# Optimization experiments

Hardware: AMD Instinct MI355X
Metric: run time of the kernel (lower is better)

## Reference

```python
import jax, jax.numpy as jnp
import numpy as np

N_NODES = 20000
N_EDGES = 400000
IN_DIM = 512
OUT_DIM = 1
HIDDEN = [512, 512, 512, 256, OUT_DIM]


def _glorot(key, fan_in, fan_out):
    lim = np.sqrt(6.0 / (fan_in + fan_out)).astype(np.float32)
    return jax.random.uniform(key, (fan_in, fan_out), jnp.float32, -lim, lim)


def setup_inputs() -> dict:
    key = jax.random.key(0)
    ks = jax.random.split(key, 16)
    x = jax.random.normal(ks[0], (N_NODES, IN_DIM), jnp.float32)
    edge_index = jax.random.randint(ks[1], (2, N_EDGES), 0, N_NODES, jnp.int64)
    edge_attr = jax.random.uniform(ks[2], (N_EDGES,), jnp.float32)
    inp = {"x": x, "edge_index": edge_index, "edge_attr": edge_attr}
    dims = [IN_DIM] + HIDDEN
    for i in range(5):
        inp[f"W{i+1}"] = _glorot(ks[3 + i], dims[i], dims[i + 1])
        inp[f"b{i+1}"] = jnp.zeros((dims[i + 1],), jnp.float32)
    return inp


def gcn_layer(x, W, b, src, dst, ew, n):
    # x: [N, Fin] -> [N, Fout]; GCNConv: D^{-1/2}(A+I)D^{-1/2} X W + b
    h = x @ W
    loop = jnp.arange(n)
    src_f = jnp.concatenate([src, loop])
    dst_f = jnp.concatenate([dst, loop])
    ew_f = jnp.concatenate([ew, jnp.ones((n,), x.dtype)])  # self-loop weight 1
    deg = jax.ops.segment_sum(ew_f, dst_f, num_segments=n)
    dinv = jnp.where(deg > 0, jax.lax.rsqrt(deg), 0.0)
    norm = dinv[src_f] * ew_f * dinv[dst_f]  # [E+N]
    out = jax.ops.segment_sum(norm[:, None] * h[src_f], dst_f, num_segments=n)
    return out + b


def reference(x, edge_index, edge_attr, W1, b1, W2, b2, W3, b3, W4, b4, W5, b5):
    src, dst = edge_index[0], edge_index[1]
    n = x.shape[0]
    h = jax.nn.relu(gcn_layer(x, W1, b1, src, dst, edge_attr, n))
    h = jax.nn.relu(gcn_layer(h, W2, b2, src, dst, edge_attr, n))
    h = jax.nn.relu(gcn_layer(h, W3, b3, src, dst, edge_attr, n))
    h = jax.nn.relu(gcn_layer(h, W4, b4, src, dst, edge_attr, n))
    h = gcn_layer(h, W5, b5, src, dst, edge_attr, n)
    return h
```

## Files before the change

### kernel.cpp

```cpp
#include <hip/hip_runtime.h>
#include <cstdint>
#include <cstddef>

#define N_NODES 20000
#define N_EDGES 400000
#define NBLK 79
#define MPAD 20128

typedef __attribute__((ext_vector_type(8))) short bf16x8;
typedef __attribute__((ext_vector_type(4))) float f32x4;

__device__ __forceinline__ float bf2f(unsigned short u) {
    return __uint_as_float(((unsigned int)u) << 16);
}
__device__ __forceinline__ unsigned short f2bf(float f) {
    unsigned int x = __float_as_uint(f);
    unsigned int lsb = (x >> 16) & 1u;
    x += 0x7fffu + lsb;
    return (unsigned short)(x >> 16);
}

__device__ __forceinline__ float ldF(const void* p, size_t i, bool bf) {
    return bf ? bf2f(((const unsigned short*)p)[i]) : ((const float*)p)[i];
}

__device__ __forceinline__ void gl2lds16(const unsigned short* g, unsigned short* l) {
    __builtin_amdgcn_global_load_lds(
        (const __attribute__((address_space(1))) void*)g,
        (__attribute__((address_space(3))) void*)l, 16, 0, 0);
}

__global__ void k_detect(const unsigned int* __restrict__ xw, const int* __restrict__ raw,
                         int* __restrict__ flag) {
    int lane = threadIdx.x;
    int cnt = 0, nz = 0;
    for (int i = lane; i < 256; i += 64) {
        unsigned short lo = (unsigned short)(xw[i] & 0xffffu);
        int e = (lo >> 7) & 0xff;
        if (e >= 110 && e <= 135) cnt++;
    }
    for (int i = 2 * lane + 1; i < 512; i += 128)
        if (raw[i] != 0) nz++;
#pragma unroll
    for (int off = 32; off > 0; off >>= 1) {
        cnt += __shfl_down(cnt, off);
        nz  += __shfl_down(nz, off);
    }
    if (lane == 0) {
        flag[0] = (cnt >= 128) ? 1 : 0;
        flag[1] = (nz == 0) ? 1 : 0;
    }
}

__global__ void k_canon_deg(const int* __restrict__ raw, const void* __restrict__ ew,
                            const int* __restrict__ flagp,
                            int* __restrict__ src32, int* __restrict__ dst32,
                            float* __restrict__ deg, int* __restrict__ counts) {
    bool bf = (flagp[0] != 0);
    int is64 = flagp[1];
    int e = blockIdx.x * blockDim.x + threadIdx.x;
    if (e >= N_EDGES) return;
    int s, d;
    if (is64) { s = raw[2 * e]; d = raw[2 * (N_EDGES + e)]; }
    else      { s = raw[e];     d = raw[N_EDGES + e]; }
    src32[e] = s;
    dst32[e] = d;
    atomicAdd(&deg[d], ldF(ew, e, bf));
    atomicAdd(&counts[d], 1);
}

__global__ __launch_bounds__(256) void k_part(const int* __restrict__ counts,
                                              const float* __restrict__ deg,
                                              float* __restrict__ dinv,
                                              float* __restrict__ selfnorm,
                                              int* __restrict__ bsum) {
    __shared__ int s[256];
    int t = threadIdx.x;
    int i = blockIdx.x * 256 + t;
    int c = (i < N_NODES) ? counts[i] : 0;
    if (i < N_NODES) {
        float d = deg[i] + 1.0f;
        float r = rsqrtf(d);
        dinv[i] = r;
        selfnorm[i] = r * r;
    }
    s[t] = c;
    __syncthreads();
    for (int off = 128; off > 0; off >>= 1) {
        if (t < off) s[t] += s[t + off];
        __syncthreads();
    }
    if (t == 0) bsum[blockIdx.x] = s[0];
}

__global__ void k_scanb(const int* __restrict__ bsum, int* __restrict__ bofs,
                        int* __restrict__ rowptr) {
    __shared__ int s[128];
    int t = threadIdx.x;
    int v = (t < NBLK) ? bsum[t] : 0;
    s[t] = v;
    __syncthreads();
    for (int off = 1; off < 128; off <<= 1) {
        int u = (t >= off) ? s[t - off] : 0;
        __syncthreads();
        s[t] += u;
        __syncthreads();
    }
    if (t < NBLK) bofs[t] = s[t] - v;
    if (t == NBLK - 1) rowptr[N_NODES] = s[t];
}

__global__ __launch_bounds__(256) void k_row(const int* __restrict__ counts,
                                             const int* __restrict__ bofs,
                                             int* __restrict__ rowptr) {
    __shared__ int s[256];
    int t = threadIdx.x;
    int b = blockIdx.x;
    int i = b * 256 + t;
    int c = (i < N_NODES) ? counts[i] : 0;
    s[t] = c;
    __syncthreads();
    for (int off = 1; off < 256; off <<= 1) {
        int u = (t >= off) ? s[t - off] : 0;
        __syncthreads();
        s[t] += u;
        __syncthreads();
    }
    if (i < N_NODES) rowptr[i] = bofs[b] + s[t] - c;
}

__global__ void k_csr(const int* __restrict__ src, const int* __restrict__ dst,
                      const void* __restrict__ ew, const int* __restrict__ flagp,
                      const float* __restrict__ dinv, const int* __restrict__ rowptr,
                      int* __restrict__ fill, int* __restrict__ csr_src,
                      float* __restrict__ csr_norm) {
    bool bf = (*flagp != 0);
    int e = blockIdx.x * blockDim.x + threadIdx.x;
    if (e >= N_EDGES) return;
    int s = src[e], d = dst[e];
    int p = rowptr[d] + atomicAdd(&fill[d], 1);
    csr_src[p] = s;
    csr_norm[p] = dinv[s] * ldF(ew, e, bf) * dinv[d];
}

__global__ __launch_bounds__(256) void k_prep(const void* __restrict__ x,
                                              const void* __restrict__ W1,
                                              const void* __restrict__ W2,
                                              const void* __restrict__ W3,
                                              const void* __restrict__ W4,
                                              const void* __restrict__ b1,
                                              const void* __restrict__ b2,
                                              const void* __restrict__ b3,
                                              const void* __restrict__ b4,
                                              const void* __restrict__ W5,
                                              const int* __restrict__ flagp,
                                              unsigned short* __restrict__ P,
                                              unsigned short* __restrict__ Wp,
                                              float* __restrict__ biasf) {
    bool bf = (*flagp != 0);
    int b = blockIdx.x;
    int t = threadIdx.x;
    if (b < 10000) {
        int i = b * 256 + t;
        if (bf) {
            ((uint2*)P)[i] = ((const uint2*)x)[i];
        } else {
            float4 v = ((const float4*)x)[i];
            unsigned int lo = (unsigned int)f2bf(v.x) | ((unsigned int)f2bf(v.y) << 16);
            unsigned int hi = (unsigned int)f2bf(v.z) | ((unsigned int)f2bf(v.w) << 16);
            ((uint2*)P)[i] = make_uint2(lo, hi);
        }
    } else if (b < 10448) {
        int gidx = (b - 10000) * 256 + t;
        if (gidx >= 114688) return;
        const void* W;
        int idx = gidx, N, nbl;
        if (gidx < 32768)      { W = W1; N = 512; nbl = 5; }
        else if (gidx < 65536) { W = W2; N = 512; nbl = 5; idx -= 32768; }
        else if (gidx < 98304) { W = W3; N = 512; nbl = 5; idx -= 65536; }
        else                   { W = W4; N = 256; nbl = 4; idx -= 98304; }
        int lane = idx & 63;
        int blk = idx >> 6;
        int nb = blk & ((1 << nbl) - 1);
        int kb = blk >> nbl;
        int n = (nb << 4) + (lane & 15);
        int kbase = (kb << 5) + ((lane >> 4) << 3);
        unsigned short o[8];
#pragma unroll
        for (int j = 0; j < 8; ++j)
            o[j] = f2bf(ldF(W, (size_t)(kbase + j) * N + n, bf));
        *(uint4*)(&Wp[(size_t)gidx * 8]) = *(const uint4*)o;
    } else {
        int i = (b - 10448) * 256 + t;
        if (i >= 2304) return;
        if (i < 2048) {
            int L = i >> 9, r = i & 511;
            if (L == 3 && r >= 256) return;
            const void* bb = (L == 0) ? b1 : (L == 1) ? b2 : (L == 2) ? b3 : b4;
            biasf[i] = ldF(bb, r, bf);
        } else {
            biasf[i] = ldF(W5, i - 2048, bf);
        }
    }
}

__global__ __launch_bounds__(256) void k_gemm_mfma(const unsigned short* __restrict__ A,
                                                   const unsigned short* __restrict__ Bp,
                                                   unsigned short* __restrict__ C,
                                                   int M, int K, int N) {
    const int AP = 72;
    __shared__ __align__(16) unsigned short As[128 * AP];
    __shared__ __align__(16) unsigned short Bs[2 * 8 * 512];
    int tid = threadIdx.x;
    int lane = tid & 63;
    int wave = tid >> 6;
    int wr = wave >> 1, wc = wave & 1;
    int row0 = blockIdx.x * 128;
    int col0 = blockIdx.y * 128;
    int nbt = N >> 4;
    int q = lane >> 4;
    int mm = lane & 15;

    f32x4 acc[4][4] = {};

    for (int kb2 = 0; kb2 < (K >> 6); ++kb2) {
        const unsigned short* breg0 = Bp + (((size_t)(2 * kb2) * nbt + (col0 >> 4)) << 9);
        const unsigned short* breg1 = Bp + (((size_t)(2 * kb2 + 1) * nbt + (col0 >> 4)) << 9);
        gl2lds16(breg0 + (size_t)tid * 8, &Bs[(size_t)tid * 8]);
        gl2lds16(breg0 + (size_t)(tid + 256) * 8, &Bs[(size_t)(tid + 256) * 8]);
        gl2lds16(breg1 + (size_t)tid * 8, &Bs[4096 + (size_t)tid * 8]);
        gl2lds16(breg1 + (size_t)(tid + 256) * 8, &Bs[4096 + (size_t)(tid + 256) * 8]);
#pragma unroll
        for (int i = 0; i < 4; ++i) {
            int c = tid + i * 256;
            int row = c >> 3, kq = c & 7;
            uint4 v = *(const uint4*)(&A[(size_t)(row0 + row) * K + (kb2 << 6) + (kq << 3)]);
            *(uint4*)(&As[row * AP + (kq << 3)]) = v;
        }
        __syncthreads();
#pragma unroll
        for (int kk = 0; kk < 2; ++kk) {
            bf16x8 af[4], bfr[4];
#pragma unroll
            for (int mb = 0; mb < 4; ++mb)
                af[mb] = *(const bf16x8*)(&As[(wr * 64 + mb * 16 + mm) * AP + kk * 32 + q * 8]);
#pragma unroll
            for (int nb = 0; nb < 4; ++nb)
                bfr[nb] = *(const bf16x8*)(&Bs[kk * 4096 + ((wc * 4 + nb) * 64 + lane) * 8]);
#pragma unroll
            for (int mb = 0; mb < 4; ++mb)
#pragma unroll
                for (int nb = 0; nb < 4; ++nb)
                    acc[mb][nb] = __builtin_amdgcn_mfma_f32_16x16x32_bf16(
                        af[mb], bfr[nb], acc[mb][nb], 0, 0, 0);
        }
        __syncthreads();
    }
#pragma unroll
    for (int mb = 0; mb < 4; ++mb) {
#pragma unroll
        for (int r = 0; r < 4; ++r) {
            int grow = row0 + wr * 64 + mb * 16 + q * 4 + r;
            if (grow < M) {
#pragma unroll
                for (int nb = 0; nb < 4; ++nb) {
                    int gcol = col0 + wc * 64 + nb * 16 + mm;
                    C[(size_t)grow * N + gcol] = f2bf(acc[mb][nb][r]);
                }
            }
        }
    }
}

template <int W>
__device__ __forceinline__ void ldrow(const unsigned short* h, size_t row, int F, int lane,
                                      unsigned int* u) {
    const unsigned int* p = (const unsigned int*)(h + row * F) + lane * W;
    if constexpr (W == 4) {
        uint4 v = *(const uint4*)p; u[0] = v.x; u[1] = v.y; u[2] = v.z; u[3] = v.w;
    } else {
        uint2 v = *(const uint2*)p; u[0] = v.x; u[1] = v.y;
    }
}
template <int W>
__device__ __forceinline__ void fmarow(const unsigned int* u, float w, float* acc) {
#pragma unroll
    for (int k = 0; k < W; ++k) {
        acc[2 * k]     = fmaf(bf2f((unsigned short)(u[k] & 0xffffu)), w, acc[2 * k]);
        acc[2 * k + 1] = fmaf(bf2f((unsigned short)(u[k] >> 16)),     w, acc[2 * k + 1]);
    }
}

__global__ __launch_bounds__(256) void k_agg_w(const unsigned short* __restrict__ h,
                                               const int* __restrict__ rowptr,
                                               const int* __restrict__ csr_src,
                                               const float* __restrict__ csr_norm,
                                               const float* __restrict__ selfnorm,
                                               const float* __restrict__ biasf,
                                               unsigned short* __restrict__ out) {
    constexpr int F = 512, FPL = 8, W = 4;
    int lane = threadIdx.x & 63;
    int wave = threadIdx.x >> 6;
    int node = blockIdx.x * 4 + wave;
    if (node >= N_NODES) return;
    int e0 = rowptr[node], e1 = rowptr[node + 1];
    float sn = selfnorm[node];

    float acc[FPL];
    {
        unsigned int u[W];
        ldrow<W>(h, (size_t)node, F, lane, u);
#pragma unroll
        for (int k = 0; k < W; ++k) {
            acc[2 * k]     = sn * bf2f((unsigned short)(u[k] & 0xffffu));
            acc[2 * k + 1] = sn * bf2f((unsigned short)(u[k] >> 16));
        }
    }
    int j = e0;
    for (; j + 3 < e1; j += 4) {
        int s0 = csr_src[j], s1 = csr_src[j + 1], s2 = csr_src[j + 2], s3 = csr_src[j + 3];
        float w0 = csr_norm[j], w1 = csr_norm[j + 1], w2 = csr_norm[j + 2], w3 = csr_norm[j + 3];
        unsigned int u0[W], u1[W], u2[W], u3[W];
        ldrow<W>(h, (size_t)s0, F, lane, u0);
        ldrow<W>(h, (size_t)s1, F, lane, u1);
        ldrow<W>(h, (size_t)s2, F, lane, u2);
        ldrow<W>(h, (size_t)s3, F, lane, u3);
        fmarow<W>(u0, w0, acc);
        fmarow<W>(u1, w1, acc);
        fmarow<W>(u2, w2, acc);
        fmarow<W>(u3, w3, acc);
    }
    for (; j < e1; ++j) {
        int s0 = csr_src[j];
        float w0 = csr_norm[j];
        unsigned int u0[W];
        ldrow<W>(h, (size_t)s0, F, lane, u0);
        fmarow<W>(u0, w0, acc);
    }
    {
        const float* bp = biasf + lane * FPL;
#pragma unroll
        for (int k = 0; k < FPL; ++k) acc[k] = fmaxf(acc[k] + bp[k], 0.f);
        unsigned int o[W];
#pragma unroll
        for (int k = 0; k < W; ++k)
            o[k] = (unsigned int)f2bf(acc[2 * k]) | ((unsigned int)f2bf(acc[2 * k + 1]) << 16);
        *(uint4*)((unsigned int*)(out + (size_t)node * F) + lane * W) =
            make_uint4(o[0], o[1], o[2], o[3]);
    }
}

__global__ __launch_bounds__(256) void k_agg_fuse(const unsigned short* __restrict__ h,
                                                  const int* __restrict__ rowptr,
                                                  const int* __restrict__ csr_src,
                                                  const float* __restrict__ csr_norm,
                                                  const float* __restrict__ selfnorm,
                                                  const float* __restrict__ biasf,
                                                  const float* __restrict__ w5f,
                                                  float* __restrict__ h5) {
    constexpr int F = 256, FPL = 4, W = 2;
    int lane = threadIdx.x & 63;
    int wave = threadIdx.x >> 6;
    int node = blockIdx.x * 4 + wave;
    if (node >= N_NODES) return;
    int e0 = rowptr[node], e1 = rowptr[node + 1];
    float sn = selfnorm[node];

    float acc[FPL];
    {
        unsigned int u[W];
        ldrow<W>(h, (size_t)node, F, lane, u);
#pragma unroll
        for (int k = 0; k < W; ++k) {
            acc[2 * k]     = sn * bf2f((unsigned short)(u[k] & 0xffffu));
            acc[2 * k + 1] = sn * bf2f((unsigned short)(u[k] >> 16));
        }
    }
    int j = e0;
    for (; j + 3 < e1; j += 4) {
        int s0 = csr_src[j], s1 = csr_src[j + 1], s2 = csr_src[j + 2], s3 = csr_src[j + 3];
        float w0 = csr_norm[j], w1 = csr_norm[j + 1], w2 = csr_norm[j + 2], w3 = csr_norm[j + 3];
        unsigned int u0[W], u1[W], u2[W], u3[W];
        ldrow<W>(h, (size_t)s0, F, lane, u0);
        ldrow<W>(h, (size_t)s1, F, lane, u1);
        ldrow<W>(h, (size_t)s2, F, lane, u2);
        ldrow<W>(h, (size_t)s3, F, lane, u3);
        fmarow<W>(u0, w0, acc);
        fmarow<W>(u1, w1, acc);
        fmarow<W>(u2, w2, acc);
        fmarow<W>(u3, w3, acc);
    }
    for (; j < e1; ++j) {
        int s0 = csr_src[j];
        float w0 = csr_norm[j];
        unsigned int u0[W];
        ldrow<W>(h, (size_t)s0, F, lane, u0);
        fmarow<W>(u0, w0, acc);
    }
    const float* bp = biasf + lane * FPL;
    const float* wp = w5f + lane * FPL;
    float partial = 0.f;
#pragma unroll
    for (int k = 0; k < FPL; ++k)
        partial += fmaxf(acc[k] + bp[k], 0.f) * wp[k];
#pragma unroll
    for (int off = 32; off > 0; off >>= 1)
        partial += __shfl_xor(partial, off);
    if (lane == 0) h5[node] = partial;
}

__global__ void k_final(const float* __restrict__ h5, const int* __restrict__ rowptr,
                        const int* __restrict__ csr_src, const float* __restrict__ csr_norm,
                        const float* __restrict__ selfnorm,
                        const void* __restrict__ b5, const int* __restrict__ flagp,
                        void* __restrict__ out) {
    bool bf = (*flagp != 0);
    int i = blockIdx.x * blockDim.x + threadIdx.x;
    if (i >= N_NODES) return;
    float acc = selfnorm[i] * h5[i];
    int e0 = rowptr[i], e1 = rowptr[i + 1];
    for (int j = e0; j < e1; ++j) acc += csr_norm[j] * h5[csr_src[j]];
    acc += ldF(b5, 0, bf);
    if (bf) ((unsigned short*)out)[i] = f2bf(acc);
    else    ((float*)out)[i] = acc;
}

extern "C" void kernel_launch(void* const* d_in, const int* in_sizes, int n_in,
                              void* d_out, int out_size, void* d_ws, size_t ws_size,
                              hipStream_t stream) {
    const void* x  = d_in[0];
    const int*  ei = (const int*)d_in[1];
    const void* ea = d_in[2];
    const void* W1 = d_in[3];
    const void* b1 = d_in[4];
    const void* W2 = d_in[5];
    const void* b2 = d_in[6];
    const void* W3 = d_in[7];
    const void* b3 = d_in[8];
    const void* W4 = d_in[9];
    const void* b4 = d_in[10];
    const void* W5 = d_in[11];
    const void* b5 = d_in[12];

    char* ws = (char*)d_ws;
    size_t off = 0;
    auto take = [&](size_t bytes) -> void* {
        off = (off + 255) & ~(size_t)255;
        void* p = ws + off;
        off += bytes;
        return p;
    };
    int*   flagp    = (int*)take(2 * sizeof(int));
    float* deg      = (float*)take(N_NODES * sizeof(float));
    int*   counts   = (int*)take(N_NODES * sizeof(int));
    int*   fill     = (int*)take(N_NODES * sizeof(int));
    size_t zspan    = (size_t)((char*)(fill + N_NODES) - (char*)deg);
    float* dinv     = (float*)take(N_NODES * sizeof(float));
    float* selfnorm = (float*)take(N_NODES * sizeof(float));
    float* h5       = (float*)take(N_NODES * sizeof(float));
    float* biasf    = (float*)take(2304 * sizeof(float));
    int*   bsum     = (int*)take(128 * sizeof(int));
    int*   bofs     = (int*)take(128 * sizeof(int));
    int*   rowptr   = (int*)take((N_NODES + 1) * sizeof(int));
    int*   src32    = (int*)take(N_EDGES * sizeof(int));
    int*   dst32    = (int*)take(N_EDGES * sizeof(int));
    int*   csr_src  = (int*)take(N_EDGES * sizeof(int));
    float* csr_norm = (float*)take(N_EDGES * sizeof(float));
    unsigned short* Wp = (unsigned short*)take((size_t)114688 * 8 * sizeof(unsigned short));
    unsigned short* P  = (unsigned short*)take((size_t)MPAD * 512 * sizeof(unsigned short));
    unsigned short* H  = (unsigned short*)take((size_t)MPAD * 512 * sizeof(unsigned short));

    hipMemsetAsync(deg, 0, zspan, stream);

    const int EB = (N_EDGES + 255) / 256;
    const int NB = (N_NODES + 255) / 256;
    const int AGB = (N_NODES + 3) / 4;

    k_detect<<<1, 64, 0, stream>>>((const unsigned int*)x, ei, flagp);
    k_canon_deg<<<EB, 256, 0, stream>>>(ei, ea, flagp, src32, dst32, deg, counts);
    k_part<<<NB, 256, 0, stream>>>(counts, deg, dinv, selfnorm, bsum);
    k_scanb<<<1, 128, 0, stream>>>(bsum, bofs, rowptr);
    k_row<<<NB, 256, 0, stream>>>(counts, bofs, rowptr);
    k_csr<<<EB, 256, 0, stream>>>(src32, dst32, ea, flagp, dinv, rowptr, fill, csr_src, csr_norm);

    k_prep<<<10457, 256, 0, stream>>>(x, W1, W2, W3, W4, b1, b2, b3, b4, W5, flagp,
                                      P, Wp, biasf);

    const int MB128 = (N_NODES + 127) / 128;

    k_gemm_mfma<<<dim3(MB128, 4), 256, 0, stream>>>(P, Wp, H, N_NODES, 512, 512);
    k_agg_w<<<AGB, 256, 0, stream>>>(H, rowptr, csr_src, csr_norm, selfnorm, biasf, P);
    k_gemm_mfma<<<dim3(MB128, 4), 256, 0, stream>>>(P, Wp + (size_t)32768 * 8, H,
                                                    N_NODES, 512, 512);
    k_agg_w<<<AGB, 256, 0, stream>>>(H, rowptr, csr_src, csr_norm, selfnorm, biasf + 512, P);
    k_gemm_mfma<<<dim3(MB128, 4), 256, 0, stream>>>(P, Wp + (size_t)65536 * 8, H,
                                                    N_NODES, 512, 512);
    k_agg_w<<<AGB, 256, 0, stream>>>(H, rowptr, csr_src, csr_norm, selfnorm, biasf + 1024, P);
    k_gemm_mfma<<<dim3(MB128, 2), 256, 0, stream>>>(P, Wp + (size_t)98304 * 8, H,
                                                    N_NODES, 512, 256);
    k_agg_fuse<<<AGB, 256, 0, stream>>>(H, rowptr, csr_src, csr_norm, selfnorm,
                                        biasf + 1536, biasf + 2048, h5);

    k_final<<<NB, 256, 0, stream>>>(h5, rowptr, csr_src, csr_norm, selfnorm, b5, flagp,
                                    d_out);
}
```

Baseline: 458.5 us.

## Split GCN aggregation across feature chunks and edge groups per wave

```diff
diff --git a/kernel.cpp b/kernel.cpp
--- a/kernel.cpp
+++ b/kernel.cpp
@@ -9,6 +9,7 @@
 
 typedef __attribute__((ext_vector_type(8))) short bf16x8;
 typedef __attribute__((ext_vector_type(4))) float f32x4;
+typedef __attribute__((ext_vector_type(2))) unsigned int u32x2;
 
 __device__ __forceinline__ float bf2f(unsigned short u) {
     return __uint_as_float(((unsigned int)u) << 16);
@@ -272,25 +273,6 @@
     }
 }
 
-template <int W>
-__device__ __forceinline__ void ldrow(const unsigned short* h, size_t row, int F, int lane,
-                                      unsigned int* u) {
-    const unsigned int* p = (const unsigned int*)(h + row * F) + lane * W;
-    if constexpr (W == 4) {
-        uint4 v = *(const uint4*)p; u[0] = v.x; u[1] = v.y; u[2] = v.z; u[3] = v.w;
-    } else {
-        uint2 v = *(const uint2*)p; u[0] = v.x; u[1] = v.y;
-    }
-}
-template <int W>
-__device__ __forceinline__ void fmarow(const unsigned int* u, float w, float* acc) {
-#pragma unroll
-    for (int k = 0; k < W; ++k) {
-        acc[2 * k]     = fmaf(bf2f((unsigned short)(u[k] & 0xffffu)), w, acc[2 * k]);
-        acc[2 * k + 1] = fmaf(bf2f((unsigned short)(u[k] >> 16)),     w, acc[2 * k + 1]);
-    }
-}
-
 __global__ __launch_bounds__(256) void k_agg_w(const unsigned short* __restrict__ h,
                                                const int* __restrict__ rowptr,
                                                const int* __restrict__ csr_src,
@@ -298,55 +280,66 @@
                                                const float* __restrict__ selfnorm,
                                                const float* __restrict__ biasf,
                                                unsigned short* __restrict__ out) {
-    constexpr int F = 512, FPL = 8, W = 4;
+    constexpr int F = 512;
     int lane = threadIdx.x & 63;
     int wave = threadIdx.x >> 6;
-    int node = blockIdx.x * 4 + wave;
+    int chunk = blockIdx.x & 7;
+    int node = (blockIdx.x >> 3) * 4 + wave;
     if (node >= N_NODES) return;
+    int r = lane >> 4;
+    int fq = lane & 15;
     int e0 = rowptr[node], e1 = rowptr[node + 1];
-    float sn = selfnorm[node];
-
-    float acc[FPL];
-    {
-        unsigned int u[W];
-        ldrow<W>(h, (size_t)node, F, lane, u);
-#pragma unroll
-        for (int k = 0; k < W; ++k) {
-            acc[2 * k]     = sn * bf2f((unsigned short)(u[k] & 0xffffu));
-            acc[2 * k + 1] = sn * bf2f((unsigned short)(u[k] >> 16));
-        }
-    }
-    int j = e0;
-    for (; j + 3 < e1; j += 4) {
-        int s0 = csr_src[j], s1 = csr_src[j + 1], s2 = csr_src[j + 2], s3 = csr_src[j + 3];
-        float w0 = csr_norm[j], w1 = csr_norm[j + 1], w2 = csr_norm[j + 2], w3 = csr_norm[j + 3];
-        unsigned int u0[W], u1[W], u2[W], u3[W];
-        ldrow<W>(h, (size_t)s0, F, lane, u0);
-        ldrow<W>(h, (size_t)s1, F, lane, u1);
-        ldrow<W>(h, (size_t)s2, F, lane, u2);
-        ldrow<W>(h, (size_t)s3, F, lane, u3);
-        fmarow<W>(u0, w0, acc);
-        fmarow<W>(u1, w1, acc);
-        fmarow<W>(u2, w2, acc);
-        fmarow<W>(u3, w3, acc);
-    }
-    for (; j < e1; ++j) {
-        int s0 = csr_src[j];
-        float w0 = csr_norm[j];
-        unsigned int u0[W];
-        ldrow<W>(h, (size_t)s0, F, lane, u0);
-        fmarow<W>(u0, w0, acc);
-    }
-    {
-        const float* bp = biasf + lane * FPL;
-#pragma unroll
-        for (int k = 0; k < FPL; ++k) acc[k] = fmaxf(acc[k] + bp[k], 0.f);
-        unsigned int o[W];
-#pragma unroll
-        for (int k = 0; k < W; ++k)
-            o[k] = (unsigned int)f2bf(acc[2 * k]) | ((unsigned int)f2bf(acc[2 * k + 1]) << 16);
-        *(uint4*)((unsigned int*)(out + (size_t)node * F) + lane * W) =
-            make_uint4(o[0], o[1], o[2], o[3]);
+    const unsigned short* hb = h + chunk * 64 + fq * 4;
+
+    float a0 = 0.f, a1 = 0.f, a2 = 0.f, a3 = 0.f;
+    if (r == 0) {
+        float sn = selfnorm[node];
+        uint2 u = *(const uint2*)(hb + (size_t)node * F);
+        a0 = sn * bf2f((unsigned short)(u.x & 0xffffu));
+        a1 = sn * bf2f((unsigned short)(u.x >> 16));
+        a2 = sn * bf2f((unsigned short)(u.y & 0xffffu));
+        a3 = sn * bf2f((unsigned short)(u.y >> 16));
+    }
+    int j = e0 + r;
+    for (; j + 4 < e1; j += 8) {
+        int s0 = __builtin_nontemporal_load(csr_src + j);
+        int s1 = __builtin_nontemporal_load(csr_src + j + 4);
+        float w0 = __builtin_nontemporal_load(csr_norm + j);
+        float w1 = __builtin_nontemporal_load(csr_norm + j + 4);
+        uint2 u0 = *(const uint2*)(hb + (size_t)s0 * F);
+        uint2 u1 = *(const uint2*)(hb + (size_t)s1 * F);
+        a0 = fmaf(bf2f((unsigned short)(u0.x & 0xffffu)), w0, a0);
+        a1 = fmaf(bf2f((unsigned short)(u0.x >> 16)),     w0, a1);
+        a2 = fmaf(bf2f((unsigned short)(u0.y & 0xffffu)), w0, a2);
+        a3 = fmaf(bf2f((unsigned short)(u0.y >> 16)),     w0, a3);
+        a0 = fmaf(bf2f((unsigned short)(u1.x & 0xffffu)), w1, a0);
+        a1 = fmaf(bf2f((unsigned short)(u1.x >> 16)),     w1, a1);
+        a2 = fmaf(bf2f((unsigned short)(u1.y & 0xffffu)), w1, a2);
+        a3 = fmaf(bf2f((unsigned short)(u1.y >> 16)),     w1, a3);
+    }
+    if (j < e1) {
+        int s0 = __builtin_nontemporal_load(csr_src + j);
+        float w0 = __builtin_nontemporal_load(csr_norm + j);
+        uint2 u0 = *(const uint2*)(hb + (size_t)s0 * F);
+        a0 = fmaf(bf2f((unsigned short)(u0.x & 0xffffu)), w0, a0);
+        a1 = fmaf(bf2f((unsigned short)(u0.x >> 16)),     w0, a1);
+        a2 = fmaf(bf2f((unsigned short)(u0.y & 0xffffu)), w0, a2);
+        a3 = fmaf(bf2f((unsigned short)(u0.y >> 16)),     w0, a3);
+    }
+    a0 += __shfl_xor(a0, 16); a0 += __shfl_xor(a0, 32);
+    a1 += __shfl_xor(a1, 16); a1 += __shfl_xor(a1, 32);
+    a2 += __shfl_xor(a2, 16); a2 += __shfl_xor(a2, 32);
+    a3 += __shfl_xor(a3, 16); a3 += __shfl_xor(a3, 32);
+    if (lane < 16) {
+        const float* bp = biasf + chunk * 64 + fq * 4;
+        a0 = fmaxf(a0 + bp[0], 0.f);
+        a1 = fmaxf(a1 + bp[1], 0.f);
+        a2 = fmaxf(a2 + bp[2], 0.f);
+        a3 = fmaxf(a3 + bp[3], 0.f);
+        u32x2 o;
+        o.x = (unsigned int)f2bf(a0) | ((unsigned int)f2bf(a1) << 16);
+        o.y = (unsigned int)f2bf(a2) | ((unsigned int)f2bf(a3) << 16);
+        __builtin_nontemporal_store(o, (u32x2*)(out + (size_t)node * F + chunk * 64 + fq * 4));
     }
 }
 
@@ -358,55 +351,66 @@
                                                   const float* __restrict__ biasf,
                                                   const float* __restrict__ w5f,
                                                   float* __restrict__ h5) {
-    constexpr int F = 256, FPL = 4, W = 2;
+    constexpr int F = 256;
     int lane = threadIdx.x & 63;
     int wave = threadIdx.x >> 6;
-    int node = blockIdx.x * 4 + wave;
+    int chunk = blockIdx.x & 7;
+    int node = (blockIdx.x >> 3) * 4 + wave;
     if (node >= N_NODES) return;
+    int rg = lane >> 3;
+    int fq = lane & 7;
     int e0 = rowptr[node], e1 = rowptr[node + 1];
-    float sn = selfnorm[node];
-
-    float acc[FPL];
-    {
-        unsigned int u[W];
-        ldrow<W>(h, (size_t)node, F, lane, u);
-#pragma unroll
-        for (int k = 0; k < W; ++k) {
-            acc[2 * k]     = sn * bf2f((unsigned short)(u[k] & 0xffffu));
-            acc[2 * k + 1] = sn * bf2f((unsigned short)(u[k] >> 16));
-        }
-    }
-    int j = e0;
-    for (; j + 3 < e1; j += 4) {
-        int s0 = csr_src[j], s1 = csr_src[j + 1], s2 = csr_src[j + 2], s3 = csr_src[j + 3];
-        float w0 = csr_norm[j], w1 = csr_norm[j + 1], w2 = csr_norm[j + 2], w3 = csr_norm[j + 3];
-        unsigned int u0[W], u1[W], u2[W], u3[W];
-        ldrow<W>(h, (size_t)s0, F, lane, u0);
-        ldrow<W>(h, (size_t)s1, F, lane, u1);
-        ldrow<W>(h, (size_t)s2, F, lane, u2);
-        ldrow<W>(h, (size_t)s3, F, lane, u3);
-        fmarow<W>(u0, w0, acc);
-        fmarow<W>(u1, w1, acc);
-        fmarow<W>(u2, w2, acc);
-        fmarow<W>(u3, w3, acc);
-    }
-    for (; j < e1; ++j) {
-        int s0 = csr_src[j];
-        float w0 = csr_norm[j];
-        unsigned int u0[W];
-        ldrow<W>(h, (size_t)s0, F, lane, u0);
-        fmarow<W>(u0, w0, acc);
-    }
-    const float* bp = biasf + lane * FPL;
-    const float* wp = w5f + lane * FPL;
-    float partial = 0.f;
-#pragma unroll
-    for (int k = 0; k < FPL; ++k)
-        partial += fmaxf(acc[k] + bp[k], 0.f) * wp[k];
-#pragma unroll
-    for (int off = 32; off > 0; off >>= 1)
-        partial += __shfl_xor(partial, off);
-    if (lane == 0) h5[node] = partial;
+    const unsigned short* hb = h + chunk * 32 + fq * 4;
+
+    float a0 = 0.f, a1 = 0.f, a2 = 0.f, a3 = 0.f;
+    if (rg == 0) {
+        float sn = selfnorm[node];
+        uint2 u = *(const uint2*)(hb + (size_t)node * F);
+        a0 = sn * bf2f((unsigned short)(u.x & 0xffffu));
+        a1 = sn * bf2f((unsigned short)(u.x >> 16));
+        a2 = sn * bf2f((unsigned short)(u.y & 0xffffu));
+        a3 = sn * bf2f((unsigned short)(u.y >> 16));
+    }
+    int j = e0 + rg;
+    for (; j + 8 < e1; j += 16) {
+        int s0 = __builtin_nontemporal_load(csr_src + j);
+        int s1 = __builtin_nontemporal_load(csr_src + j + 8);
+        float w0 = __builtin_nontemporal_load(csr_norm + j);
+        float w1 = __builtin_nontemporal_load(csr_norm + j + 8);
+        uint2 u0 = *(const uint2*)(hb + (size_t)s0 * F);
+        uint2 u1 = *(const uint2*)(hb + (size_t)s1 * F);
+        a0 = fmaf(bf2f((unsigned short)(u0.x & 0xffffu)), w0, a0);
+        a1 = fmaf(bf2f((unsigned short)(u0.x >> 16)),     w0, a1);
+        a2 = fmaf(bf2f((unsigned short)(u0.y & 0xffffu)), w0, a2);
+        a3 = fmaf(bf2f((unsigned short)(u0.y >> 16)),     w0, a3);
+        a0 = fmaf(bf2f((unsigned short)(u1.x & 0xffffu)), w1, a0);
+        a1 = fmaf(bf2f((unsigned short)(u1.x >> 16)),     w1, a1);
+        a2 = fmaf(bf2f((unsigned short)(u1.y & 0xffffu)), w1, a2);
+        a3 = fmaf(bf2f((unsigned short)(u1.y >> 16)),     w1, a3);
+    }
+    if (j < e1) {
+        int s0 = __builtin_nontemporal_load(csr_src + j);
+        float w0 = __builtin_nontemporal_load(csr_norm + j);
+        uint2 u0 = *(const uint2*)(hb + (size_t)s0 * F);
+        a0 = fmaf(bf2f((unsigned short)(u0.x & 0xffffu)), w0, a0);
+        a1 = fmaf(bf2f((unsigned short)(u0.x >> 16)),     w0, a1);
+        a2 = fmaf(bf2f((unsigned short)(u0.y & 0xffffu)), w0, a2);
+        a3 = fmaf(bf2f((unsigned short)(u0.y >> 16)),     w0, a3);
+    }
+    a0 += __shfl_xor(a0, 8); a0 += __shfl_xor(a0, 16); a0 += __shfl_xor(a0, 32);
+    a1 += __shfl_xor(a1, 8); a1 += __shfl_xor(a1, 16); a1 += __shfl_xor(a1, 32);
+    a2 += __shfl_xor(a2, 8); a2 += __shfl_xor(a2, 16); a2 += __shfl_xor(a2, 32);
+    a3 += __shfl_xor(a3, 8); a3 += __shfl_xor(a3, 16); a3 += __shfl_xor(a3, 32);
+    const float* bp = biasf + chunk * 32 + fq * 4;
+    const float* wp = w5f + chunk * 32 + fq * 4;
+    float partial = fmaxf(a0 + bp[0], 0.f) * wp[0]
+                  + fmaxf(a1 + bp[1], 0.f) * wp[1]
+                  + fmaxf(a2 + bp[2], 0.f) * wp[2]
+                  + fmaxf(a3 + bp[3], 0.f) * wp[3];
+    partial += __shfl_xor(partial, 1);
+    partial += __shfl_xor(partial, 2);
+    partial += __shfl_xor(partial, 4);
+    if (lane == 0) atomicAdd(h5 + node, partial);
 }
 
 __global__ void k_final(const float* __restrict__ h5, const int* __restrict__ rowptr,
@@ -454,10 +458,10 @@
     float* deg      = (float*)take(N_NODES * sizeof(float));
     int*   counts   = (int*)take(N_NODES * sizeof(int));
     int*   fill     = (int*)take(N_NODES * sizeof(int));
-    size_t zspan    = (size_t)((char*)(fill + N_NODES) - (char*)deg);
+    float* h5       = (float*)take(N_NODES * sizeof(float));
+    size_t zspan    = (size_t)((char*)(h5 + N_NODES) - (char*)deg);
     float* dinv     = (float*)take(N_NODES * sizeof(float));
     float* selfnorm = (float*)take(N_NODES * sizeof(float));
-    float* h5       = (float*)take(N_NODES * sizeof(float));
     float* biasf    = (float*)take(2304 * sizeof(float));
     int*   bsum     = (int*)take(128 * sizeof(int));
     int*   bofs     = (int*)take(128 * sizeof(int));
@@ -470,11 +474,11 @@
     unsigned short* P  = (unsigned short*)take((size_t)MPAD * 512 * sizeof(unsigned short));
     unsigned short* H  = (unsigned short*)take((size_t)MPAD * 512 * sizeof(unsigned short));
 
-    hipMemsetAsync(deg, 0, zspan, stream);
+    (void)hipMemsetAsync(deg, 0, zspan, stream);
 
     const int EB = (N_EDGES + 255) / 256;
     const int NB = (N_NODES + 255) / 256;
-    const int AGB = (N_NODES + 3) / 4;
+    const int AGBC = ((N_NODES + 3) / 4) * 8;
 
     k_detect<<<1, 64, 0, stream>>>((const unsigned int*)x, ei, flagp);
     k_canon_deg<<<EB, 256, 0, stream>>>(ei, ea, flagp, src32, dst32, deg, counts);
@@ -489,17 +493,17 @@
     const int MB128 = (N_NODES + 127) / 128;
 
     k_gemm_mfma<<<dim3(MB128, 4), 256, 0, stream>>>(P, Wp, H, N_NODES, 512, 512);
-    k_agg_w<<<AGB, 256, 0, stream>>>(H, rowptr, csr_src, csr_norm, selfnorm, biasf, P);
+    k_agg_w<<<AGBC, 256, 0, stream>>>(H, rowptr, csr_src, csr_norm, selfnorm, biasf, P);
     k_gemm_mfma<<<dim3(MB128, 4), 256, 0, stream>>>(P, Wp + (size_t)32768 * 8, H,
                                                     N_NODES, 512, 512);
-    k_agg_w<<<AGB, 256, 0, stream>>>(H, rowptr, csr_src, csr_norm, selfnorm, biasf + 512, P);
+    k_agg_w<<<AGBC, 256, 0, stream>>>(H, rowptr, csr_src, csr_norm, selfnorm, biasf + 512, P);
     k_gemm_mfma<<<dim3(MB128, 4), 256, 0, stream>>>(P, Wp + (size_t)65536 * 8, H,
                                                     N_NODES, 512, 512);
-    k_agg_w<<<AGB, 256, 0, stream>>>(H, rowptr, csr_src, csr_norm, selfnorm, biasf + 1024, P);
+    k_agg_w<<<AGBC, 256, 0, stream>>>(H, rowptr, csr_src, csr_norm, selfnorm, biasf + 1024, P);
     k_gemm_mfma<<<dim3(MB128, 2), 256, 0, stream>>>(P, Wp + (size_t)98304 * 8, H,
                                                     N_NODES, 512, 256);
-    k_agg_fuse<<<AGB, 256, 0, stream>>>(H, rowptr, csr_src, csr_norm, selfnorm,
-                                        biasf + 1536, biasf + 2048, h5);
+    k_agg_fuse<<<AGBC, 256, 0, stream>>>(H, rowptr, csr_src, csr_norm, selfnorm,
+                                         biasf + 1536, biasf + 2048, h5);
 
     k_final<<<NB, 256, 0, stream>>>(h5, rowptr, csr_src, csr_norm, selfnorm, b5, flagp,
                                     d_out);
```

After: 654.6 us. +42.8%, slower.

## Split aggregation into feature chunks with edge-parallel groups and packed CSR pairs

Applied to the files above, without the earlier changes.

```diff
diff --git a/kernel.cpp b/kernel.cpp
--- a/kernel.cpp
+++ b/kernel.cpp
@@ -9,6 +9,8 @@
 
 typedef __attribute__((ext_vector_type(8))) short bf16x8;
 typedef __attribute__((ext_vector_type(4))) float f32x4;
+typedef __attribute__((ext_vector_type(2))) int i32x2;
+typedef __attribute__((ext_vector_type(4))) unsigned int u32x4;
 
 __device__ __forceinline__ float bf2f(unsigned short u) {
     return __uint_as_float(((unsigned int)u) << 16);
@@ -28,6 +30,17 @@
     __builtin_amdgcn_global_load_lds(
         (const __attribute__((address_space(1))) void*)g,
         (__attribute__((address_space(3))) void*)l, 16, 0, 0);
+}
+
+__device__ __forceinline__ void fma8(float* acc, const uint4& u, float w) {
+    acc[0] = fmaf(bf2f((unsigned short)(u.x & 0xffffu)), w, acc[0]);
+    acc[1] = fmaf(bf2f((unsigned short)(u.x >> 16)),     w, acc[1]);
+    acc[2] = fmaf(bf2f((unsigned short)(u.y & 0xffffu)), w, acc[2]);
+    acc[3] = fmaf(bf2f((unsigned short)(u.y >> 16)),     w, acc[3]);
+    acc[4] = fmaf(bf2f((unsigned short)(u.z & 0xffffu)), w, acc[4]);
+    acc[5] = fmaf(bf2f((unsigned short)(u.z >> 16)),     w, acc[5]);
+    acc[6] = fmaf(bf2f((unsigned short)(u.w & 0xffffu)), w, acc[6]);
+    acc[7] = fmaf(bf2f((unsigned short)(u.w >> 16)),     w, acc[7]);
 }
 
 __global__ void k_detect(const unsigned int* __restrict__ xw, const int* __restrict__ raw,
@@ -132,15 +145,17 @@
 __global__ void k_csr(const int* __restrict__ src, const int* __restrict__ dst,
                       const void* __restrict__ ew, const int* __restrict__ flagp,
                       const float* __restrict__ dinv, const int* __restrict__ rowptr,
-                      int* __restrict__ fill, int* __restrict__ csr_src,
-                      float* __restrict__ csr_norm) {
+                      int* __restrict__ fill, int* __restrict__ csr_pair) {
     bool bf = (*flagp != 0);
     int e = blockIdx.x * blockDim.x + threadIdx.x;
     if (e >= N_EDGES) return;
     int s = src[e], d = dst[e];
     int p = rowptr[d] + atomicAdd(&fill[d], 1);
-    csr_src[p] = s;
-    csr_norm[p] = dinv[s] * ldF(ew, e, bf) * dinv[d];
+    float nrm = dinv[s] * ldF(ew, e, bf) * dinv[d];
+    i32x2 pv;
+    pv.x = s;
+    pv.y = __float_as_int(nrm);
+    *(i32x2*)(csr_pair + 2 * (size_t)p) = pv;
 }
 
 __global__ __launch_bounds__(256) void k_prep(const void* __restrict__ x,
@@ -272,145 +287,155 @@
     }
 }
 
-template <int W>
-__device__ __forceinline__ void ldrow(const unsigned short* h, size_t row, int F, int lane,
-                                      unsigned int* u) {
-    const unsigned int* p = (const unsigned int*)(h + row * F) + lane * W;
-    if constexpr (W == 4) {
-        uint4 v = *(const uint4*)p; u[0] = v.x; u[1] = v.y; u[2] = v.z; u[3] = v.w;
-    } else {
-        uint2 v = *(const uint2*)p; u[0] = v.x; u[1] = v.y;
-    }
-}
-template <int W>
-__device__ __forceinline__ void fmarow(const unsigned int* u, float w, float* acc) {
-#pragma unroll
-    for (int k = 0; k < W; ++k) {
-        acc[2 * k]     = fmaf(bf2f((unsigned short)(u[k] & 0xffffu)), w, acc[2 * k]);
-        acc[2 * k + 1] = fmaf(bf2f((unsigned short)(u[k] >> 16)),     w, acc[2 * k + 1]);
-    }
-}
-
 __global__ __launch_bounds__(256) void k_agg_w(const unsigned short* __restrict__ h,
                                                const int* __restrict__ rowptr,
-                                               const int* __restrict__ csr_src,
-                                               const float* __restrict__ csr_norm,
+                                               const int* __restrict__ csr_pair,
                                                const float* __restrict__ selfnorm,
                                                const float* __restrict__ biasf,
                                                unsigned short* __restrict__ out) {
-    constexpr int F = 512, FPL = 8, W = 4;
+    constexpr int F = 512;
     int lane = threadIdx.x & 63;
     int wave = threadIdx.x >> 6;
-    int node = blockIdx.x * 4 + wave;
+    int chunk = blockIdx.x & 7;
+    int node = (blockIdx.x >> 3) * 4 + wave;
     if (node >= N_NODES) return;
+    int g = lane >> 3;
+    int fl = lane & 7;
     int e0 = rowptr[node], e1 = rowptr[node + 1];
-    float sn = selfnorm[node];
-
-    float acc[FPL];
-    {
-        unsigned int u[W];
-        ldrow<W>(h, (size_t)node, F, lane, u);
-#pragma unroll
-        for (int k = 0; k < W; ++k) {
-            acc[2 * k]     = sn * bf2f((unsigned short)(u[k] & 0xffffu));
-            acc[2 * k + 1] = sn * bf2f((unsigned short)(u[k] >> 16));
-        }
-    }
-    int j = e0;
-    for (; j + 3 < e1; j += 4) {
-        int s0 = csr_src[j], s1 = csr_src[j + 1], s2 = csr_src[j + 2], s3 = csr_src[j + 3];
-        float w0 = csr_norm[j], w1 = csr_norm[j + 1], w2 = csr_norm[j + 2], w3 = csr_norm[j + 3];
-        unsigned int u0[W], u1[W], u2[W], u3[W];
-        ldrow<W>(h, (size_t)s0, F, lane, u0);
-        ldrow<W>(h, (size_t)s1, F, lane, u1);
-        ldrow<W>(h, (size_t)s2, F, lane, u2);
-        ldrow<W>(h, (size_t)s3, F, lane, u3);
-        fmarow<W>(u0, w0, acc);
-        fmarow<W>(u1, w1, acc);
-        fmarow<W>(u2, w2, acc);
-        fmarow<W>(u3, w3, acc);
-    }
-    for (; j < e1; ++j) {
-        int s0 = csr_src[j];
-        float w0 = csr_norm[j];
-        unsigned int u0[W];
-        ldrow<W>(h, (size_t)s0, F, lane, u0);
-        fmarow<W>(u0, w0, acc);
-    }
-    {
-        const float* bp = biasf + lane * FPL;
-#pragma unroll
-        for (int k = 0; k < FPL; ++k) acc[k] = fmaxf(acc[k] + bp[k], 0.f);
-        unsigned int o[W];
-#pragma unroll
-        for (int k = 0; k < W; ++k)
-            o[k] = (unsigned int)f2bf(acc[2 * k]) | ((unsigned int)f2bf(acc[2 * k + 1]) << 16);
-        *(uint4*)((unsigned int*)(out + (size_t)node * F) + lane * W) =
-            make_uint4(o[0], o[1], o[2], o[3]);
+    const unsigned short* hb = h + chunk * 64 + fl * 8;
+
+    float acc[8] = {};
+    if (g == 0) {
+        float sn = selfnorm[node];
+        uint4 u = *(const uint4*)(hb + (size_t)node * F);
+        fma8(acc, u, sn);
+    }
+    for (int base = e0; base < e1; base += 64) {
+        int nb = min(64, e1 - base);
+        int ps = 0, pwb = 0;
+        if (lane < nb) {
+            i32x2 pv = __builtin_nontemporal_load((const i32x2*)csr_pair + (base + lane));
+            ps = pv.x;
+            pwb = pv.y;
+        }
+        int nbat = (nb + 7) >> 3;
+        int m = g;
+        bool ok = m < nb;
+        int mm0 = ok ? m : 0;
+        int s_cur = __shfl(ps, mm0);
+        float w_cur = __uint_as_float((unsigned int)__shfl(pwb, mm0));
+        if (!ok) w_cur = 0.f;
+        uint4 u_cur = *(const uint4*)(hb + (size_t)s_cur * F);
+        for (int t = 1; t < nbat; ++t) {
+            int m2 = t * 8 + g;
+            bool ok2 = m2 < nb;
+            int mm2 = ok2 ? m2 : 0;
+            int s_n = __shfl(ps, mm2);
+            float w_n = __uint_as_float((unsigned int)__shfl(pwb, mm2));
+            if (!ok2) w_n = 0.f;
+            uint4 u_n = *(const uint4*)(hb + (size_t)s_n * F);
+            fma8(acc, u_cur, w_cur);
+            u_cur = u_n;
+            w_cur = w_n;
+        }
+        fma8(acc, u_cur, w_cur);
+    }
+#pragma unroll
+    for (int k = 0; k < 8; ++k) {
+        acc[k] += __shfl_xor(acc[k], 8);
+        acc[k] += __shfl_xor(acc[k], 16);
+        acc[k] += __shfl_xor(acc[k], 32);
+    }
+    if (g == 0) {
+        const float* bp = biasf + chunk * 64 + fl * 8;
+        u32x4 o;
+        unsigned int ow[4];
+#pragma unroll
+        for (int k = 0; k < 4; ++k) {
+            float lo = fmaxf(acc[2 * k]     + bp[2 * k],     0.f);
+            float hi = fmaxf(acc[2 * k + 1] + bp[2 * k + 1], 0.f);
+            ow[k] = (unsigned int)f2bf(lo) | ((unsigned int)f2bf(hi) << 16);
+        }
+        o.x = ow[0]; o.y = ow[1]; o.z = ow[2]; o.w = ow[3];
+        __builtin_nontemporal_store(
+            o, (u32x4*)(out + (size_t)node * F + chunk * 64 + fl * 8));
     }
 }
 
 __global__ __launch_bounds__(256) void k_agg_fuse(const unsigned short* __restrict__ h,
                                                   const int* __restrict__ rowptr,
-                                                  const int* __restrict__ csr_src,
-                                                  const float* __restrict__ csr_norm,
+                                                  const int* __restrict__ csr_pair,
                                                   const float* __restrict__ selfnorm,
                                                   const float* __restrict__ biasf,
                                                   const float* __restrict__ w5f,
                                                   float* __restrict__ h5) {
-    constexpr int F = 256, FPL = 4, W = 2;
+    constexpr int F = 256;
     int lane = threadIdx.x & 63;
     int wave = threadIdx.x >> 6;
-    int node = blockIdx.x * 4 + wave;
+    int chunk = blockIdx.x & 3;
+    int node = (blockIdx.x >> 2) * 4 + wave;
     if (node >= N_NODES) return;
+    int g = lane >> 3;
+    int fl = lane & 7;
     int e0 = rowptr[node], e1 = rowptr[node + 1];
-    float sn = selfnorm[node];
-
-    float acc[FPL];
-    {
-        unsigned int u[W];
-        ldrow<W>(h, (size_t)node, F, lane, u);
-#pragma unroll
-        for (int k = 0; k < W; ++k) {
-            acc[2 * k]     = sn * bf2f((unsigned short)(u[k] & 0xffffu));
-            acc[2 * k + 1] = sn * bf2f((unsigned short)(u[k] >> 16));
-        }
-    }
-    int j = e0;
-    for (; j + 3 < e1; j += 4) {
-        int s0 = csr_src[j], s1 = csr_src[j + 1], s2 = csr_src[j + 2], s3 = csr_src[j + 3];
-        float w0 = csr_norm[j], w1 = csr_norm[j + 1], w2 = csr_norm[j + 2], w3 = csr_norm[j + 3];
-        unsigned int u0[W], u1[W], u2[W], u3[W];
-        ldrow<W>(h, (size_t)s0, F, lane, u0);
-        ldrow<W>(h, (size_t)s1, F, lane, u1);
-        ldrow<W>(h, (size_t)s2, F, lane, u2);
-        ldrow<W>(h, (size_t)s3, F, lane, u3);
-        fmarow<W>(u0, w0, acc);
-        fmarow<W>(u1, w1, acc);
-        fmarow<W>(u2, w2, acc);
-        fmarow<W>(u3, w3, acc);
-    }
-    for (; j < e1; ++j) {
-        int s0 = csr_src[j];
-        float w0 = csr_norm[j];
-        unsigned int u0[W];
-        ldrow<W>(h, (size_t)s0, F, lane, u0);
-        fmarow<W>(u0, w0, acc);
-    }
-    const float* bp = biasf + lane * FPL;
-    const float* wp = w5f + lane * FPL;
+    const unsigned short* hb = h + chunk * 64 + fl * 8;
+
+    float acc[8] = {};
+    if (g == 0) {
+        float sn = selfnorm[node];
+        uint4 u = *(const uint4*)(hb + (size_t)node * F);
+        fma8(acc, u, sn);
+    }
+    for (int base = e0; base < e1; base += 64) {
+        int nb = min(64, e1 - base);
+        int ps = 0, pwb = 0;
+        if (lane < nb) {
+            i32x2 pv = __builtin_nontemporal_load((const i32x2*)csr_pair + (base + lane));
+            ps = pv.x;
+            pwb = pv.y;
+        }
+        int nbat = (nb + 7) >> 3;
+        int m = g;
+        bool ok = m < nb;
+        int mm0 = ok ? m : 0;
+        int s_cur = __shfl(ps, mm0);
+        float w_cur = __uint_as_float((unsigned int)__shfl(pwb, mm0));
+        if (!ok) w_cur = 0.f;
+        uint4 u_cur = *(const uint4*)(hb + (size_t)s_cur * F);
+        for (int t = 1; t < nbat; ++t) {
+            int m2 = t * 8 + g;
+            bool ok2 = m2 < nb;
+            int mm2 = ok2 ? m2 : 0;
+            int s_n = __shfl(ps, mm2);
+            float w_n = __uint_as_float((unsigned int)__shfl(pwb, mm2));
+            if (!ok2) w_n = 0.f;
+            uint4 u_n = *(const uint4*)(hb + (size_t)s_n * F);
+            fma8(acc, u_cur, w_cur);
+            u_cur = u_n;
+            w_cur = w_n;
+        }
+        fma8(acc, u_cur, w_cur);
+    }
+#pragma unroll
+    for (int k = 0; k < 8; ++k) {
+        acc[k] += __shfl_xor(acc[k], 8);
+        acc[k] += __shfl_xor(acc[k], 16);
+        acc[k] += __shfl_xor(acc[k], 32);
+    }
+    const float* bp = biasf + chunk * 64 + fl * 8;
+    const float* wp = w5f + chunk * 64 + fl * 8;
     float partial = 0.f;
 #pragma unroll
-    for (int k = 0; k < FPL; ++k)
+    for (int k = 0; k < 8; ++k)
         partial += fmaxf(acc[k] + bp[k], 0.f) * wp[k];
-#pragma unroll
-    for (int off = 32; off > 0; off >>= 1)
-        partial += __shfl_xor(partial, off);
-    if (lane == 0) h5[node] = partial;
+    partial += __shfl_xor(partial, 1);
+    partial += __shfl_xor(partial, 2);
+    partial += __shfl_xor(partial, 4);
+    if (lane == 0) atomicAdd(h5 + node, partial);
 }
 
 __global__ void k_final(const float* __restrict__ h5, const int* __restrict__ rowptr,
-                        const int* __restrict__ csr_src, const float* __restrict__ csr_norm,
+                        const int* __restrict__ csr_pair,
                         const float* __restrict__ selfnorm,
                         const void* __restrict__ b5, const int* __restrict__ flagp,
                         void* __restrict__ out) {
@@ -419,7 +444,11 @@
     if (i >= N_NODES) return;
     float acc = selfnorm[i] * h5[i];
     int e0 = rowptr[i], e1 = rowptr[i + 1];
-    for (int j = e0; j < e1; ++j) acc += csr_norm[j] * h5[csr_src[j]];
+    for (int j = e0; j < e1; ++j) {
+        int s = csr_pair[2 * (size_t)j];
+        float w = __int_as_float(csr_pair[2 * (size_t)j + 1]);
+        acc += w * h5[s];
+    }
     acc += ldF(b5, 0, bf);
     if (bf) ((unsigned short*)out)[i] = f2bf(acc);
     else    ((float*)out)[i] = acc;
@@ -454,34 +483,34 @@
     float* deg      = (float*)take(N_NODES * sizeof(float));
     int*   counts   = (int*)take(N_NODES * sizeof(int));
     int*   fill     = (int*)take(N_NODES * sizeof(int));
-    size_t zspan    = (size_t)((char*)(fill + N_NODES) - (char*)deg);
+    float* h5       = (float*)take(N_NODES * sizeof(float));
+    size_t zspan    = (size_t)((char*)(h5 + N_NODES) - (char*)deg);
     float* dinv     = (float*)take(N_NODES * sizeof(float));
     float* selfnorm = (float*)take(N_NODES * sizeof(float));
-    float* h5       = (float*)take(N_NODES * sizeof(float));
     float* biasf    = (float*)take(2304 * sizeof(float));
     int*   bsum     = (int*)take(128 * sizeof(int));
     int*   bofs     = (int*)take(128 * sizeof(int));
     int*   rowptr   = (int*)take((N_NODES + 1) * sizeof(int));
     int*   src32    = (int*)take(N_EDGES * sizeof(int));
     int*   dst32    = (int*)take(N_EDGES * sizeof(int));
-    int*   csr_src  = (int*)take(N_EDGES * sizeof(int));
-    float* csr_norm = (float*)take(N_EDGES * sizeof(float));
+    int*   csr_pair = (int*)take((size_t)N_EDGES * 2 * sizeof(int));
     unsigned short* Wp = (unsigned short*)take((size_t)114688 * 8 * sizeof(unsigned short));
     unsigned short* P  = (unsigned short*)take((size_t)MPAD * 512 * sizeof(unsigned short));
     unsigned short* H  = (unsigned short*)take((size_t)MPAD * 512 * sizeof(unsigned short));
 
-    hipMemsetAsync(deg, 0, zspan, stream);
+    (void)hipMemsetAsync(deg, 0, zspan, stream);
 
     const int EB = (N_EDGES + 255) / 256;
     const int NB = (N_NODES + 255) / 256;
-    const int AGB = (N_NODES + 3) / 4;
+    const int AGBC = ((N_NODES + 3) / 4) * 8;
+    const int AGF  = ((N_NODES + 3) / 4) * 4;
 
     k_detect<<<1, 64, 0, stream>>>((const unsigned int*)x, ei, flagp);
     k_canon_deg<<<EB, 256, 0, stream>>>(ei, ea, flagp, src32, dst32, deg, counts);
     k_part<<<NB, 256, 0, stream>>>(counts, deg, dinv, selfnorm, bsum);
     k_scanb<<<1, 128, 0, stream>>>(bsum, bofs, rowptr);
     k_row<<<NB, 256, 0, stream>>>(counts, bofs, rowptr);
-    k_csr<<<EB, 256, 0, stream>>>(src32, dst32, ea, flagp, dinv, rowptr, fill, csr_src, csr_norm);
+    k_csr<<<EB, 256, 0, stream>>>(src32, dst32, ea, flagp, dinv, rowptr, fill, csr_pair);
 
     k_prep<<<10457, 256, 0, stream>>>(x, W1, W2, W3, W4, b1, b2, b3, b4, W5, flagp,
                                       P, Wp, biasf);
@@ -489,18 +518,18 @@
     const int MB128 = (N_NODES + 127) / 128;
 
     k_gemm_mfma<<<dim3(MB128, 4), 256, 0, stream>>>(P, Wp, H, N_NODES, 512, 512);
-    k_agg_w<<<AGB, 256, 0, stream>>>(H, rowptr, csr_src, csr_norm, selfnorm, biasf, P);
+    k_agg_w<<<AGBC, 256, 0, stream>>>(H, rowptr, csr_pair, selfnorm, biasf, P);
     k_gemm_mfma<<<dim3(MB128, 4), 256, 0, stream>>>(P, Wp + (size_t)32768 * 8, H,
                                                     N_NODES, 512, 512);
-    k_agg_w<<<AGB, 256, 0, stream>>>(H, rowptr, csr_src, csr_norm, selfnorm, biasf + 512, P);
+    k_agg_w<<<AGBC, 256, 0, stream>>>(H, rowptr, csr_pair, selfnorm, biasf + 512, P);
     k_gemm_mfma<<<dim3(MB128, 4), 256, 0, stream>>>(P, Wp + (size_t)65536 * 8, H,
                                                     N_NODES, 512, 512);
-    k_agg_w<<<AGB, 256, 0, stream>>>(H, rowptr, csr_src, csr_norm, selfnorm, biasf + 1024, P);
+    k_agg_w<<<AGBC, 256, 0, stream>>>(H, rowptr, csr_pair, selfnorm, biasf + 1024, P);
     k_gemm_mfma<<<dim3(MB128, 2), 256, 0, stream>>>(P, Wp + (size_t)98304 * 8, H,
                                                     N_NODES, 512, 256);
-    k_agg_fuse<<<AGB, 256, 0, stream>>>(H, rowptr, csr_src, csr_norm, selfnorm,
+    k_agg_fuse<<<AGF, 256, 0, stream>>>(H, rowptr, csr_pair, selfnorm,
                                         biasf + 1536, biasf + 2048, h5);
 
-    k_final<<<NB, 256, 0, stream>>>(h5, rowptr, csr_src, csr_norm, selfnorm, b5, flagp,
+    k_final<<<NB, 256, 0, stream>>>(h5, rowptr, csr_pair, selfnorm, b5, flagp,
                                     d_out);
 }
```

Measured after the change: 554.9 us. 1.21x slower.
